# Optimization experiments

Measured on AMD Instinct MI355X. Metric: run time of the kernel, lower is better.

Reference implementation:

```python
import jax, jax.numpy as jnp
import numpy as np

N = 6            # fixed by nn.Linear(6, h2) after the transpose/squeeze
NEG_SLOPE = 0.01 # F.leaky_relu default


def setup_inputs() -> dict:
    key = jax.random.key(0)
    ks = jax.random.split(key, 12)
    B, H1, H2, H3 = 131072, 64, 512, 256
    in_feat = jax.random.normal(ks[0], (N, B, 1), dtype=jnp.float32)
    # deterministic bidirectional ring: every node has in/out degree 2 (norm='both' safe)
    ar = jnp.arange(N, dtype=jnp.int32)
    src = jnp.concatenate([ar, ar])
    dst = jnp.concatenate([(ar + 1) % N, (ar - 1) % N]).astype(jnp.int32)
    s = 0.2
    W0  = jax.random.normal(ks[1], (1, H1), jnp.float32) * s
    b0  = jax.random.normal(ks[2], (H1,), jnp.float32) * s
    W1  = jax.random.normal(ks[3], (H1, 1), jnp.float32) * s
    b1  = jax.random.normal(ks[4], (1,), jnp.float32) * s
    Wl0 = jax.random.normal(ks[5], (N, H2), jnp.float32) * s
    bl0 = jax.random.normal(ks[6], (H2,), jnp.float32) * s
    Wl2 = jax.random.normal(ks[7], (H2, H3), jnp.float32) * s
    bl2 = jax.random.normal(ks[8], (H3,), jnp.float32) * s
    Wl3 = jax.random.normal(ks[9], (H3, 1), jnp.float32) * s
    bl3 = jax.random.normal(ks[10], (1,), jnp.float32) * s
    return {"in_feat": in_feat, "src": src, "dst": dst,
            "W0": W0, "b0": b0, "W1": W1, "b1": b1,
            "Wl0": Wl0, "bl0": bl0, "Wl2": Wl2, "bl2": bl2,
            "Wl3": Wl3, "bl3": bl3}


def _lrelu(x):
    return jnp.where(x >= 0, x, NEG_SLOPE * x)


def _degree_norms(src, dst):
    ones = jnp.ones(src.shape[0], dtype=jnp.float32)
    deg_out = jax.ops.segment_sum(ones, src, num_segments=N)
    deg_in = jax.ops.segment_sum(ones, dst, num_segments=N)
    return deg_out ** -0.5, deg_in ** -0.5  # DGL GraphConv norm='both'


def _graph_conv(feat, W, b, src, dst, inv_out, inv_in):
    # D_out^{-1/2} A^T D_in^{-1/2} feat  then linear (order is math-equivalent)
    h = feat * inv_out[:, None, None]           # [N,B,F]
    agg = jax.ops.segment_sum(h[src], dst, num_segments=N)  # gather+scatter over edges
    agg = agg * inv_in[:, None, None]
    return agg @ W + b


def reference(in_feat, src, dst, W0, b0, W1, b1, Wl0, bl0, Wl2, bl2, Wl3, bl3):
    inv_out, inv_in = _degree_norms(src, dst)
    h = _lrelu(_graph_conv(in_feat, W0, b0, src, dst, inv_out, inv_in))  # [N,B,h1]
    h = _lrelu(_graph_conv(h, W1, b1, src, dst, inv_out, inv_in))        # [N,B,1]
    x = jnp.transpose(h, (2, 1, 0))[0]   # transpose(0,2).squeeze(0) -> [B,N]
    x = _lrelu(x @ Wl0 + bl0)
    x = _lrelu(x @ Wl2 + bl2)
    x = _lrelu(x @ Wl3 + bl3)            # [B,1]; squeeze(0) is a no-op for B>1
    return x
```

## Files before the change

### kernel.cpp

```cpp
#include <hip/hip_runtime.h>

#define NN   6
#define H1   64
#define H2   512
#define H3   256
#define TM   256
#define KC   32
#define NCH  (H2 / KC)
#define CHUNK_BYTES 32768

typedef short s16x8 __attribute__((ext_vector_type(8)));
typedef float f32x16 __attribute__((ext_vector_type(16)));
typedef float f32x2 __attribute__((ext_vector_type(2)));
typedef unsigned int u32x4 __attribute__((ext_vector_type(4)));

__device__ __forceinline__ unsigned short f2bf(float x) {
    unsigned int u = __float_as_uint(x);
    u += 0x7FFFu + ((u >> 16) & 1u);
    return (unsigned short)(u >> 16);
}
__device__ __forceinline__ float bf2f(unsigned short b) {
    return __uint_as_float(((unsigned int)b) << 16);
}
__device__ __forceinline__ unsigned int cvt_pk_bf16(float a, float b) {
    unsigned int r;
    asm("v_cvt_pk_bf16_f32 %0, %1, %2" : "=v"(r) : "v"(a), "v"(b));
    return r;
}
__device__ __forceinline__ void g2lds16(const void* g, void* l) {
    __builtin_amdgcn_global_load_lds(
        (const __attribute__((address_space(1))) unsigned int*)g,
        (__attribute__((address_space(3))) unsigned int*)l, 16, 0, 0);
}

__global__ void split_w(const float* __restrict__ Wl2,
                        unsigned short* __restrict__ Whl) {
    const int gid = blockIdx.x * 256 + threadIdx.x;
    const int k = gid >> 6, c4 = (gid & 63) << 2;
    const float4 v = *(const float4*)&Wl2[k * H3 + c4];
    const int c0 = k >> 5, th = (k >> 3) & 3, j = k & 7;
    const unsigned base = (c0 << 14) + (th << 11) + j;
    const float vv[4] = {v.x, v.y, v.z, v.w};
    #pragma unroll
    for (int c = 0; c < 4; ++c) {
        const unsigned short hi = f2bf(vv[c]);
        const unsigned short lo = f2bf(vv[c] - bf2f(hi));
        Whl[base + ((c4 + c) << 3)] = hi;
        Whl[base + 8192 + ((c4 + c) << 3)] = lo;
    }
}

__device__ __forceinline__ void gen2(const float* sBl0s, const float (*sWl0s)[H2],
                                     int k0, const float* xr0, const float* xr1,
                                     s16x8& ah0, s16x8& al0, s16x8& ah1, s16x8& al1)
{
    f32x2 a0[4], a1[4];
    #pragma unroll
    for (int j = 0; j < 4; ++j) {
        const f32x2 b = *(const f32x2*)&sBl0s[k0 + 2 * j];
        f32x2 c0 = b, c1 = b;
        #pragma unroll
        for (int i = 0; i < 6; ++i) {
            const f32x2 wv = *(const f32x2*)&sWl0s[i][k0 + 2 * j];
            c0 += xr0[i] * wv;
            c1 += xr1[i] * wv;
        }
        a0[j] = c0; a1[j] = c1;
    }
    unsigned int h0[4], l0[4], h1[4], l1[4];
    #pragma unroll
    for (int j = 0; j < 4; ++j) {
        f32x2 v = a0[j];
        v = __builtin_elementwise_max(v, 0.01f * v);
        unsigned int u = cvt_pk_bf16(v[0], v[1]);
        f32x2 hf = { __uint_as_float(u << 16), __uint_as_float(u & 0xFFFF0000u) };
        f32x2 r = v - hf;
        h0[j] = u; l0[j] = cvt_pk_bf16(r[0], r[1]);
        v = a1[j];
        v = __builtin_elementwise_max(v, 0.01f * v);
        u = cvt_pk_bf16(v[0], v[1]);
        hf = (f32x2){ __uint_as_float(u << 16), __uint_as_float(u & 0xFFFF0000u) };
        r = v - hf;
        h1[j] = u; l1[j] = cvt_pk_bf16(r[0], r[1]);
    }
    u32x4 t;
    t = (u32x4){h0[0], h0[1], h0[2], h0[3]}; ah0 = __builtin_bit_cast(s16x8, t);
    t = (u32x4){l0[0], l0[1], l0[2], l0[3]}; al0 = __builtin_bit_cast(s16x8, t);
    t = (u32x4){h1[0], h1[1], h1[2], h1[3]}; ah1 = __builtin_bit_cast(s16x8, t);
    t = (u32x4){l1[0], l1[1], l1[2], l1[3]}; al1 = __builtin_bit_cast(s16x8, t);
}

__global__ __launch_bounds__(512, 2)
void gcn_mfma(const float* __restrict__ f,
              const float* __restrict__ W0,
              const float* __restrict__ b0,
              const float* __restrict__ W1,
              const float* __restrict__ b1_,
              const float* __restrict__ Wl0,
              const float* __restrict__ bl0,
              const float* __restrict__ bl2,
              const float* __restrict__ Wl3,
              const float* __restrict__ bl3_,
              const unsigned short* __restrict__ Whl,
              float* __restrict__ out,
              int B)
{
    __shared__ float sW0[H1], sB0[H1], sW1[H1];
    __shared__ float sWl0[NN][H2];
    __shared__ float sBl0[H2];
    __shared__ float sBl2[H3];
    __shared__ float sWl3[H3];
    __shared__ float sF[NN][TM];
    __shared__ float sS[NN][TM];
    __shared__ float sX[NN][TM];
    __shared__ __align__(16) unsigned short sB[2][16384];

    const int t     = threadIdx.x;
    const int lane  = t & 63;
    const int w     = t >> 6;
    const int cl    = lane & 31;
    const int h     = lane >> 5;
    const int wr    = w >> 1;
    const int wc    = w & 1;
    const int wc128 = wc << 7;
    const int m0    = blockIdx.x * TM;

    for (int i = t; i < H1; i += 512) { sW0[i] = W0[i]; sB0[i] = b0[i]; sW1[i] = W1[i]; }
    for (int i = t; i < NN * H2; i += 512) sWl0[i >> 9][i & (H2 - 1)] = Wl0[i];
    for (int i = t; i < H2; i += 512) sBl0[i] = bl0[i];
    for (int i = t; i < H3; i += 512) { sBl2[i] = bl2[i]; sWl3[i] = Wl3[i]; }
    for (int i = t; i < NN * TM; i += 512) sF[i >> 8][i & 255] = f[(i >> 8) * B + m0 + (i & 255)];

#define STAGE(CH, BUF) do {                                                        \
        const char* _src = (const char*)Whl + (CH) * CHUNK_BYTES + (w << 12) + (lane << 4); \
        char*       _dst = (char*)&sB[BUF][0] + (w << 12);                         \
        _Pragma("unroll")                                                          \
        for (int _q = 0; _q < 4; ++_q) g2lds16(_src + (_q << 10), _dst + (_q << 10)); \
    } while (0)

    STAGE(0, 0);
    __syncthreads();

    const float b1v = b1_[0];

    for (int v = t; v < NN * TM; v += 512) {
        const int i = v >> 8, r = v & 255;
        const int im = (i + NN - 1) % NN, ip = (i + 1) % NN;
        const float g = 0.5f * (sF[im][r] + sF[ip][r]);
        float s = 0.f;
        #pragma unroll
        for (int c = 0; c < H1; ++c) {
            float hx = g * sW0[c] + sB0[c];
            hx = fmaxf(hx, 0.01f * hx);
            s += hx * sW1[c];
        }
        sS[i][r] = s;
    }
    __syncthreads();
    for (int v = t; v < NN * TM; v += 512) {
        const int i = v >> 8, r = v & 255;
        const int im = (i + NN - 1) % NN, ip = (i + 1) % NN;
        const float xv = 0.5f * (sS[im][r] + sS[ip][r]) + b1v;
        sX[i][r] = fmaxf(xv, 0.01f * xv);
    }
    __syncthreads();

    const int row0 = (wr << 6) + cl;
    float xr0[NN], xr1[NN];
    #pragma unroll
    for (int i = 0; i < NN; ++i) { xr0[i] = sX[i][row0]; xr1[i] = sX[i][row0 + 32]; }

    f32x16 acc[2][4];
    #pragma unroll
    for (int m = 0; m < 2; ++m)
        #pragma unroll
        for (int n = 0; n < 4; ++n)
            #pragma unroll
            for (int rg = 0; rg < 16; ++rg) acc[m][n][rg] = 0.f;

#define K0(CH, TT) (((CH) << 5) + ((TT) << 4) + (h << 3))

#define MFMA_TT(SBC, TT, AH0, AL0, AH1, AL1) do {                                  \
        const int _thh = ((TT) << 1) + h;                                          \
        const unsigned short* _bb = &(SBC)[((_thh << 8) + wc128 + cl) << 3];       \
        s16x8 _bh[4], _bl[4];                                                      \
        _Pragma("unroll")                                                          \
        for (int _n = 0; _n < 4; ++_n) {                                           \
            _bh[_n] = *(const s16x8*)&_bb[_n << 8];                                \
            _bl[_n] = *(const s16x8*)&_bb[8192 + (_n << 8)];                       \
        }                                                                          \
        _Pragma("unroll")                                                          \
        for (int _n = 0; _n < 4; ++_n) {                                           \
            acc[0][_n] = __builtin_amdgcn_mfma_f32_32x32x16_bf16(AH0, _bh[_n], acc[0][_n], 0, 0, 0); \
            acc[1][_n] = __builtin_amdgcn_mfma_f32_32x32x16_bf16(AH1, _bh[_n], acc[1][_n], 0, 0, 0); \
            acc[0][_n] = __builtin_amdgcn_mfma_f32_32x32x16_bf16(AL0, _bh[_n], acc[0][_n], 0, 0, 0); \
            acc[1][_n] = __builtin_amdgcn_mfma_f32_32x32x16_bf16(AL1, _bh[_n], acc[1][_n], 0, 0, 0); \
            acc[0][_n] = __builtin_amdgcn_mfma_f32_32x32x16_bf16(AH0, _bl[_n], acc[0][_n], 0, 0, 0); \
            acc[1][_n] = __builtin_amdgcn_mfma_f32_32x32x16_bf16(AH1, _bl[_n], acc[1][_n], 0, 0, 0); \
        }                                                                          \
    } while (0)

    s16x8 fA[2][4], fB[2][4];
    gen2(sBl0, sWl0, K0(0, 0), xr0, xr1, fA[0][0], fA[0][1], fA[0][2], fA[0][3]);
    gen2(sBl0, sWl0, K0(0, 1), xr0, xr1, fA[1][0], fA[1][1], fA[1][2], fA[1][3]);

    for (int ch = 0; ch < NCH; ch += 2) {
        STAGE(ch + 1, 1);
        gen2(sBl0, sWl0, K0(ch + 1, 0), xr0, xr1, fB[0][0], fB[0][1], fB[0][2], fB[0][3]);
        gen2(sBl0, sWl0, K0(ch + 1, 1), xr0, xr1, fB[1][0], fB[1][1], fB[1][2], fB[1][3]);
        MFMA_TT((&sB[0][0]), 0, fA[0][0], fA[0][1], fA[0][2], fA[0][3]);
        MFMA_TT((&sB[0][0]), 1, fA[1][0], fA[1][1], fA[1][2], fA[1][3]);
        __syncthreads();
        if (ch + 2 < NCH) {
            STAGE(ch + 2, 0);
            gen2(sBl0, sWl0, K0(ch + 2, 0), xr0, xr1, fA[0][0], fA[0][1], fA[0][2], fA[0][3]);
            gen2(sBl0, sWl0, K0(ch + 2, 1), xr0, xr1, fA[1][0], fA[1][1], fA[1][2], fA[1][3]);
        }
        MFMA_TT((&sB[1][0]), 0, fB[0][0], fB[0][1], fB[0][2], fB[0][3]);
        MFMA_TT((&sB[1][0]), 1, fB[1][0], fB[1][1], fB[1][2], fB[1][3]);
        __syncthreads();
    }

    float ps[2][16];
    #pragma unroll
    for (int m = 0; m < 2; ++m)
        #pragma unroll
        for (int rg = 0; rg < 16; ++rg) ps[m][rg] = 0.f;
    #pragma unroll
    for (int m = 0; m < 2; ++m)
        #pragma unroll
        for (int n = 0; n < 4; ++n) {
            const int col = wc128 + (n << 5) + cl;
            const float b2 = sBl2[col], w3 = sWl3[col];
            #pragma unroll
            for (int rg = 0; rg < 16; ++rg) {
                float v = acc[m][n][rg] + b2;
                v = fmaxf(v, 0.01f * v);
                ps[m][rg] += v * w3;
            }
        }
    #pragma unroll
    for (int msk = 1; msk < 32; msk <<= 1)
        #pragma unroll
        for (int m = 0; m < 2; ++m)
            #pragma unroll
            for (int rg = 0; rg < 16; ++rg) ps[m][rg] += __shfl_xor(ps[m][rg], msk);

    float* sRed = &sS[0][0];
    if (cl == 0) {
        #pragma unroll
        for (int m = 0; m < 2; ++m)
            #pragma unroll
            for (int rg = 0; rg < 16; ++rg) {
                const int rowb = (wr << 6) + (m << 5) + (rg & 3) + ((rg >> 2) << 3) + (h << 2);
                sRed[(wc << 8) + rowb] = ps[m][rg];
            }
    }
    __syncthreads();
    if (t < 256) {
        const float bl3v = bl3_[0];
        const float v = sRed[t] + sRed[256 + t] + bl3v;
        out[m0 + t] = fmaxf(v, 0.01f * v);
    }
}

extern "C" void kernel_launch(void* const* d_in, const int* in_sizes, int n_in,
                              void* d_out, int out_size, void* d_ws, size_t ws_size,
                              hipStream_t stream) {
    const float* f   = (const float*)d_in[0];
    const float* W0  = (const float*)d_in[3];
    const float* b0  = (const float*)d_in[4];
    const float* W1  = (const float*)d_in[5];
    const float* b1  = (const float*)d_in[6];
    const float* Wl0 = (const float*)d_in[7];
    const float* bl0 = (const float*)d_in[8];
    const float* Wl2 = (const float*)d_in[9];
    const float* bl2 = (const float*)d_in[10];
    const float* Wl3 = (const float*)d_in[11];
    const float* bl3 = (const float*)d_in[12];
    float* out = (float*)d_out;
    unsigned short* Whl = (unsigned short*)d_ws;
    const int B = in_sizes[0] / NN;

    split_w<<<dim3(128), 256, 0, stream>>>(Wl2, Whl);
    gcn_mfma<<<dim3(B / TM), 512, 0, stream>>>(f, W0, b0, W1, b1, Wl0, bl0,
                                               bl2, Wl3, bl3, Whl, out, B);
}
```

Measured before the change: 194.4 us.

## Halve row tile and K chunk, use 256-thread blocks with new weight layout

Shrinks the row tile from 256 to 128 and the K chunk from 32 to 16, runs 4-wave blocks instead of 8-wave ones, and doubles the grid. The split-weight buffer gets a new layout written as 16-byte vectors, and the MFMA loop interleaves B-fragment loads with MFMAs in two groups. The aim is smaller LDS use, more resident blocks and finer-grained pipelining. In exchange there are twice as many barriers per unit of work, and each block reloads the weights and re-runs the GCN prologue per smaller tile.

```diff
diff --git a/kernel.cpp b/kernel.cpp
--- a/kernel.cpp
+++ b/kernel.cpp
@@ -4,10 +4,10 @@
 #define H1   64
 #define H2   512
 #define H3   256
-#define TM   256
-#define KC   32
+#define TM   128
+#define KC   16
 #define NCH  (H2 / KC)
-#define CHUNK_BYTES 32768
+#define CHUNK_BYTES 16384
 
 typedef short s16x8 __attribute__((ext_vector_type(8)));
 typedef float f32x16 __attribute__((ext_vector_type(16)));
@@ -35,19 +35,20 @@
 
 __global__ void split_w(const float* __restrict__ Wl2,
                         unsigned short* __restrict__ Whl) {
-    const int gid = blockIdx.x * 256 + threadIdx.x;
-    const int k = gid >> 6, c4 = (gid & 63) << 2;
-    const float4 v = *(const float4*)&Wl2[k * H3 + c4];
-    const int c0 = k >> 5, th = (k >> 3) & 3, j = k & 7;
-    const unsigned base = (c0 << 14) + (th << 11) + j;
-    const float vv[4] = {v.x, v.y, v.z, v.w};
-    #pragma unroll
-    for (int c = 0; c < 4; ++c) {
-        const unsigned short hi = f2bf(vv[c]);
-        const unsigned short lo = f2bf(vv[c] - bf2f(hi));
-        Whl[base + ((c4 + c) << 3)] = hi;
-        Whl[base + 8192 + ((c4 + c) << 3)] = lo;
-    }
+    const int tid = blockIdx.x * 256 + threadIdx.x;
+    const int c0 = tid >> 9, th = (tid >> 8) & 1, col = tid & 255;
+    const int kb = (c0 << 4) + (th << 3);
+    s16x8 hi8, lo8;
+    #pragma unroll
+    for (int j = 0; j < 8; ++j) {
+        const float w = Wl2[(kb + j) * H3 + col];
+        const unsigned short hi = f2bf(w);
+        hi8[j] = (short)hi;
+        lo8[j] = (short)f2bf(w - bf2f(hi));
+    }
+    const int base = (c0 << 13) + (th << 11) + (col << 3);
+    *(s16x8*)&Whl[base] = hi8;
+    *(s16x8*)&Whl[base + 4096] = lo8;
 }
 
 __device__ __forceinline__ void gen2(const float* sBl0s, const float (*sWl0s)[H2],
@@ -90,7 +91,7 @@
     t = (u32x4){l1[0], l1[1], l1[2], l1[3]}; al1 = __builtin_bit_cast(s16x8, t);
 }
 
-__global__ __launch_bounds__(512, 2)
+__global__ __launch_bounds__(256, 2)
 void gcn_mfma(const float* __restrict__ f,
               const float* __restrict__ W0,
               const float* __restrict__ b0,
@@ -113,7 +114,7 @@
     __shared__ float sF[NN][TM];
     __shared__ float sS[NN][TM];
     __shared__ float sX[NN][TM];
-    __shared__ __align__(16) unsigned short sB[2][16384];
+    __shared__ __align__(16) unsigned short sB[2][8192];
 
     const int t     = threadIdx.x;
     const int lane  = t & 63;
@@ -125,11 +126,11 @@
     const int wc128 = wc << 7;
     const int m0    = blockIdx.x * TM;
 
-    for (int i = t; i < H1; i += 512) { sW0[i] = W0[i]; sB0[i] = b0[i]; sW1[i] = W1[i]; }
-    for (int i = t; i < NN * H2; i += 512) sWl0[i >> 9][i & (H2 - 1)] = Wl0[i];
-    for (int i = t; i < H2; i += 512) sBl0[i] = bl0[i];
-    for (int i = t; i < H3; i += 512) { sBl2[i] = bl2[i]; sWl3[i] = Wl3[i]; }
-    for (int i = t; i < NN * TM; i += 512) sF[i >> 8][i & 255] = f[(i >> 8) * B + m0 + (i & 255)];
+    for (int i = t; i < H1; i += 256) { sW0[i] = W0[i]; sB0[i] = b0[i]; sW1[i] = W1[i]; }
+    for (int i = t; i < NN * H2; i += 256) sWl0[i >> 9][i & (H2 - 1)] = Wl0[i];
+    for (int i = t; i < H2; i += 256) sBl0[i] = bl0[i];
+    for (int i = t; i < H3; i += 256) { sBl2[i] = bl2[i]; sWl3[i] = Wl3[i]; }
+    for (int i = t; i < NN * TM; i += 256) sF[i >> 7][i & 127] = f[(i >> 7) * B + m0 + (i & 127)];
 
 #define STAGE(CH, BUF) do {                                                        \
         const char* _src = (const char*)Whl + (CH) * CHUNK_BYTES + (w << 12) + (lane << 4); \
@@ -143,8 +144,8 @@
 
     const float b1v = b1_[0];
 
-    for (int v = t; v < NN * TM; v += 512) {
-        const int i = v >> 8, r = v & 255;
+    for (int v = t; v < NN * TM; v += 256) {
+        const int i = v >> 7, r = v & 127;
         const int im = (i + NN - 1) % NN, ip = (i + 1) % NN;
         const float g = 0.5f * (sF[im][r] + sF[ip][r]);
         float s = 0.f;
@@ -157,8 +158,8 @@
         sS[i][r] = s;
     }
     __syncthreads();
-    for (int v = t; v < NN * TM; v += 512) {
-        const int i = v >> 8, r = v & 255;
+    for (int v = t; v < NN * TM; v += 256) {
+        const int i = v >> 7, r = v & 127;
         const int im = (i + NN - 1) % NN, ip = (i + 1) % NN;
         const float xv = 0.5f * (sS[im][r] + sS[ip][r]) + b1v;
         sX[i][r] = fmaxf(xv, 0.01f * xv);
@@ -178,46 +179,46 @@
             #pragma unroll
             for (int rg = 0; rg < 16; ++rg) acc[m][n][rg] = 0.f;
 
-#define K0(CH, TT) (((CH) << 5) + ((TT) << 4) + (h << 3))
-
-#define MFMA_TT(SBC, TT, AH0, AL0, AH1, AL1) do {                                  \
-        const int _thh = ((TT) << 1) + h;                                          \
-        const unsigned short* _bb = &(SBC)[((_thh << 8) + wc128 + cl) << 3];       \
-        s16x8 _bh[4], _bl[4];                                                      \
+#define K0(CH) (((CH) << 4) + (h << 3))
+
+#define MFMA_CH(SBC, AH0, AL0, AH1, AL1) do {                                      \
+        const unsigned short* _bb = &(SBC)[(h << 11) + ((wc128 + cl) << 3)];       \
         _Pragma("unroll")                                                          \
-        for (int _n = 0; _n < 4; ++_n) {                                           \
-            _bh[_n] = *(const s16x8*)&_bb[_n << 8];                                \
-            _bl[_n] = *(const s16x8*)&_bb[8192 + (_n << 8)];                       \
-        }                                                                          \
-        _Pragma("unroll")                                                          \
-        for (int _n = 0; _n < 4; ++_n) {                                           \
-            acc[0][_n] = __builtin_amdgcn_mfma_f32_32x32x16_bf16(AH0, _bh[_n], acc[0][_n], 0, 0, 0); \
-            acc[1][_n] = __builtin_amdgcn_mfma_f32_32x32x16_bf16(AH1, _bh[_n], acc[1][_n], 0, 0, 0); \
-            acc[0][_n] = __builtin_amdgcn_mfma_f32_32x32x16_bf16(AL0, _bh[_n], acc[0][_n], 0, 0, 0); \
-            acc[1][_n] = __builtin_amdgcn_mfma_f32_32x32x16_bf16(AL1, _bh[_n], acc[1][_n], 0, 0, 0); \
-            acc[0][_n] = __builtin_amdgcn_mfma_f32_32x32x16_bf16(AH0, _bl[_n], acc[0][_n], 0, 0, 0); \
-            acc[1][_n] = __builtin_amdgcn_mfma_f32_32x32x16_bf16(AH1, _bl[_n], acc[1][_n], 0, 0, 0); \
+        for (int _g = 0; _g < 2; ++_g) {                                           \
+            const int _o = _g << 9;                                                \
+            const s16x8 _bha = *(const s16x8*)&_bb[_o];                            \
+            const s16x8 _bhb = *(const s16x8*)&_bb[_o + 256];                      \
+            const s16x8 _bla = *(const s16x8*)&_bb[4096 + _o];                     \
+            const s16x8 _blb = *(const s16x8*)&_bb[4096 + _o + 256];               \
+            const int _n = _g << 1;                                                \
+            acc[0][_n]   = __builtin_amdgcn_mfma_f32_32x32x16_bf16(AH0, _bha, acc[0][_n],   0, 0, 0); \
+            acc[1][_n]   = __builtin_amdgcn_mfma_f32_32x32x16_bf16(AH1, _bha, acc[1][_n],   0, 0, 0); \
+            acc[0][_n+1] = __builtin_amdgcn_mfma_f32_32x32x16_bf16(AH0, _bhb, acc[0][_n+1], 0, 0, 0); \
+            acc[1][_n+1] = __builtin_amdgcn_mfma_f32_32x32x16_bf16(AH1, _bhb, acc[1][_n+1], 0, 0, 0); \
+            acc[0][_n]   = __builtin_amdgcn_mfma_f32_32x32x16_bf16(AL0, _bha, acc[0][_n],   0, 0, 0); \
+            acc[1][_n]   = __builtin_amdgcn_mfma_f32_32x32x16_bf16(AL1, _bha, acc[1][_n],   0, 0, 0); \
+            acc[0][_n+1] = __builtin_amdgcn_mfma_f32_32x32x16_bf16(AL0, _bhb, acc[0][_n+1], 0, 0, 0); \
+            acc[1][_n+1] = __builtin_amdgcn_mfma_f32_32x32x16_bf16(AL1, _bhb, acc[1][_n+1], 0, 0, 0); \
+            acc[0][_n]   = __builtin_amdgcn_mfma_f32_32x32x16_bf16(AH0, _bla, acc[0][_n],   0, 0, 0); \
+            acc[1][_n]   = __builtin_amdgcn_mfma_f32_32x32x16_bf16(AH1, _bla, acc[1][_n],   0, 0, 0); \
+            acc[0][_n+1] = __builtin_amdgcn_mfma_f32_32x32x16_bf16(AH0, _blb, acc[0][_n+1], 0, 0, 0); \
+            acc[1][_n+1] = __builtin_amdgcn_mfma_f32_32x32x16_bf16(AH1, _blb, acc[1][_n+1], 0, 0, 0); \
         }                                                                          \
     } while (0)
 
-    s16x8 fA[2][4], fB[2][4];
-    gen2(sBl0, sWl0, K0(0, 0), xr0, xr1, fA[0][0], fA[0][1], fA[0][2], fA[0][3]);
-    gen2(sBl0, sWl0, K0(0, 1), xr0, xr1, fA[1][0], fA[1][1], fA[1][2], fA[1][3]);
+    s16x8 fA[4], fB[4];
+    gen2(sBl0, sWl0, K0(0), xr0, xr1, fA[0], fA[1], fA[2], fA[3]);
 
     for (int ch = 0; ch < NCH; ch += 2) {
         STAGE(ch + 1, 1);
-        gen2(sBl0, sWl0, K0(ch + 1, 0), xr0, xr1, fB[0][0], fB[0][1], fB[0][2], fB[0][3]);
-        gen2(sBl0, sWl0, K0(ch + 1, 1), xr0, xr1, fB[1][0], fB[1][1], fB[1][2], fB[1][3]);
-        MFMA_TT((&sB[0][0]), 0, fA[0][0], fA[0][1], fA[0][2], fA[0][3]);
-        MFMA_TT((&sB[0][0]), 1, fA[1][0], fA[1][1], fA[1][2], fA[1][3]);
+        gen2(sBl0, sWl0, K0(ch + 1), xr0, xr1, fB[0], fB[1], fB[2], fB[3]);
+        MFMA_CH((&sB[0][0]), fA[0], fA[1], fA[2], fA[3]);
         __syncthreads();
         if (ch + 2 < NCH) {
             STAGE(ch + 2, 0);
-            gen2(sBl0, sWl0, K0(ch + 2, 0), xr0, xr1, fA[0][0], fA[0][1], fA[0][2], fA[0][3]);
-            gen2(sBl0, sWl0, K0(ch + 2, 1), xr0, xr1, fA[1][0], fA[1][1], fA[1][2], fA[1][3]);
-        }
-        MFMA_TT((&sB[1][0]), 0, fB[0][0], fB[0][1], fB[0][2], fB[0][3]);
-        MFMA_TT((&sB[1][0]), 1, fB[1][0], fB[1][1], fB[1][2], fB[1][3]);
+            gen2(sBl0, sWl0, K0(ch + 2), xr0, xr1, fA[0], fA[1], fA[2], fA[3]);
+        }
+        MFMA_CH((&sB[1][0]), fB[0], fB[1], fB[2], fB[3]);
         __syncthreads();
     }
 
@@ -253,13 +254,13 @@
             #pragma unroll
             for (int rg = 0; rg < 16; ++rg) {
                 const int rowb = (wr << 6) + (m << 5) + (rg & 3) + ((rg >> 2) << 3) + (h << 2);
-                sRed[(wc << 8) + rowb] = ps[m][rg];
+                sRed[(wc << 7) + rowb] = ps[m][rg];
             }
     }
     __syncthreads();
-    if (t < 256) {
+    if (t < TM) {
         const float bl3v = bl3_[0];
-        const float v = sRed[t] + sRed[256 + t] + bl3v;
+        const float v = sRed[t] + sRed[TM + t] + bl3v;
         out[m0 + t] = fmaxf(v, 0.01f * v);
     }
 }
@@ -282,7 +283,7 @@
     unsigned short* Whl = (unsigned short*)d_ws;
     const int B = in_sizes[0] / NN;
 
-    split_w<<<dim3(128), 256, 0, stream>>>(Wl2, Whl);
-    gcn_mfma<<<dim3(B / TM), 512, 0, stream>>>(f, W0, b0, W1, b1, Wl0, bl0,
+    split_w<<<dim3(64), 256, 0, stream>>>(Wl2, Whl);
+    gcn_mfma<<<dim3(B / TM), 256, 0, stream>>>(f, W0, b0, W1, b1, Wl0, bl0,
                                                bl2, Wl3, bl3, Whl, out, B);
 }
```

Measured after the change: 195.0 us. Within noise of the previous version (+0.3%).
